# Optimization experiments

Hardware: AMD Instinct MI355X
Metric: run time of the kernel (lower is better)

Reference implementation:

```python
import jax, jax.numpy as jnp
import numpy as np

N_NODES = 100000
N_EDGES = 1600000
N_GRAPHS = 4096
BN_EPS = 1e-5


def _gcn_conv(h, src, tgt, deg_inv_sqrt, W, b):
    # GCNConv with self-loops: out_i = sum_{j->i} (d_i d_j)^{-1/2} (XW)_j + d_i^{-1} (XW)_i + b
    h = h @ W                                   # [N, out]
    norm = (deg_inv_sqrt[src] * deg_inv_sqrt[tgt])[:, None]  # [E, 1]
    agg = jax.ops.segment_sum(h[src] * norm, tgt, num_segments=N_NODES)
    agg = agg + h * (deg_inv_sqrt ** 2)[:, None]  # self-loop term
    return agg + b


def _batch_norm(x, gamma, beta):
    # training-mode BatchNorm1d: batch statistics, biased variance
    mean = jnp.mean(x, axis=0)
    var = jnp.mean((x - mean) ** 2, axis=0)
    return (x - mean) * jax.lax.rsqrt(var + BN_EPS) * gamma + beta


def setup_inputs() -> dict:
    key = jax.random.key(0)
    ks = jax.random.split(key, 12)
    x = jax.random.normal(ks[0], (N_NODES, 128), dtype=jnp.float32)
    edge_index = jax.random.randint(ks[1], (2, N_EDGES), 0, N_NODES, dtype=jnp.int32)
    batch = jnp.sort(jax.random.randint(ks[2], (N_NODES,), 0, N_GRAPHS, dtype=jnp.int32))
    def lin(k, fi, fo):
        return jax.random.normal(k, (fi, fo), dtype=jnp.float32) / np.sqrt(fi)
    return {
        "x": x, "edge_index": edge_index, "batch": batch,
        "W1": lin(ks[3], 128, 128), "b1": jnp.zeros((128,), jnp.float32),
        "W2": lin(ks[4], 128, 128), "b2": jnp.zeros((128,), jnp.float32),
        "W3": lin(ks[5], 128, 256), "b3": jnp.zeros((256,), jnp.float32),
        "g1": jnp.ones((128,), jnp.float32), "be1": jnp.zeros((128,), jnp.float32),
        "g2": jnp.ones((128,), jnp.float32), "be2": jnp.zeros((128,), jnp.float32),
    }


def reference(x, edge_index, batch, W1, b1, W2, b2, W3, b3, g1, be1, g2, be2):
    src, tgt = edge_index[0], edge_index[1]
    # degrees including self-loop
    deg = jax.ops.segment_sum(jnp.ones((N_EDGES,), x.dtype), tgt, num_segments=N_NODES) + 1.0
    deg_inv_sqrt = jax.lax.rsqrt(deg)

    h = _gcn_conv(x, src, tgt, deg_inv_sqrt, W1, b1)
    h = jax.nn.relu(_batch_norm(h, g1, be1))          # dropout(p=0.1) as identity (eval)
    h = _gcn_conv(h, src, tgt, deg_inv_sqrt, W2, b2)
    h = jax.nn.relu(_batch_norm(h, g2, be2))
    h = _gcn_conv(h, src, tgt, deg_inv_sqrt, W3, b3)  # [N, 256]

    # global mean pool over batch ids
    sums = jax.ops.segment_sum(h, batch, num_segments=N_GRAPHS)
    counts = jax.ops.segment_sum(jnp.ones((N_NODES,), h.dtype), batch, num_segments=N_GRAPHS)
    return sums / jnp.maximum(counts, 1.0)[:, None]
```

## Files before the change

kernel.cpp:

```cpp
#include <hip/hip_runtime.h>
#include <hip/hip_bf16.h>

#define BN_EPS 1e-5f
#define SCAN_CHUNK 2048
#define AGG_BLOCKS 2048
#define BSHIFT 9
#define BUCKN 512
#define NBP 256
#define CB 256

static inline int cdiv(long long a, long long b) { return (int)((a + b - 1) / b); }

typedef __attribute__((ext_vector_type(8))) short short8v;
typedef __attribute__((ext_vector_type(4))) float f32x4;

__device__ __forceinline__ float lo16(int u) {
    return __uint_as_float(((unsigned int)u) << 16);
}
__device__ __forceinline__ float hi16(int u) {
    return __uint_as_float(((unsigned int)u) & 0xffff0000u);
}
__device__ __forceinline__ unsigned short f2bf(float f) {
    unsigned int b = __float_as_uint(f);
    b += 0x7FFFu + ((b >> 16) & 1u);
    return (unsigned short)(b >> 16);
}

__global__ __launch_bounds__(256) void k_bhist(const int* __restrict__ tgt,
                                               int* __restrict__ hcnt, int E, int tile,
                                               int nbuck) {
    __shared__ int lh[NBP];
    const int t = threadIdx.x;
    lh[t] = 0;
    __syncthreads();
    const int base = blockIdx.x * tile;
    const int end = min(base + tile, E);
    for (int i = base + t; i < end; i += 256)
        atomicAdd(&lh[tgt[i] >> BSHIFT], 1);
    __syncthreads();
    if (t < nbuck) hcnt[blockIdx.x * NBP + t] = lh[t];
}

__global__ __launch_bounds__(256) void k_bscan(int* __restrict__ hcnt,
                                               int* __restrict__ btot) {
    const int bucket = blockIdx.x;
    const int t = threadIdx.x;
    __shared__ int sh[256];
    int v = hcnt[t * NBP + bucket];
    sh[t] = v;
    __syncthreads();
    for (int d = 1; d < 256; d <<= 1) {
        int u = (t >= d) ? sh[t - d] : 0;
        __syncthreads();
        sh[t] += u;
        __syncthreads();
    }
    hcnt[t * NBP + bucket] = sh[t] - v;
    if (t == 255) btot[bucket] = sh[255];
}

__global__ __launch_bounds__(256) void k_scan_small(const int* __restrict__ btot,
                                                    int* __restrict__ bbase, int nb) {
    const int t = threadIdx.x;
    __shared__ int sh[256];
    int v = (t < nb) ? btot[t] : 0;
    sh[t] = v;
    __syncthreads();
    for (int d = 1; d < 256; d <<= 1) {
        int u = (t >= d) ? sh[t - d] : 0;
        __syncthreads();
        sh[t] += u;
        __syncthreads();
    }
    if (t < nb) bbase[t] = sh[t] - v;
    if (t == nb) bbase[nb] = sh[255];
    if (t == 255 && nb <= 255) bbase[nb] = sh[255];
}

__global__ __launch_bounds__(256) void k_bscatter2(const int* __restrict__ src,
                                                   const int* __restrict__ tgt,
                                                   const int* __restrict__ hcnt,
                                                   const int* __restrict__ bbase,
                                                   int2* __restrict__ pairs, int E,
                                                   int tile, int nbuck) {
    __shared__ int cur[NBP];
    const int t = threadIdx.x;
    if (t < nbuck) cur[t] = bbase[t] + hcnt[blockIdx.x * NBP + t];
    __syncthreads();
    const int base = blockIdx.x * tile;
    const int end = min(base + tile, E);
    for (int i = base + t; i < end; i += 256) {
        int s = src[i];
        int tg = tgt[i];
        int p = atomicAdd(&cur[tg >> BSHIFT], 1);
        pairs[p] = make_int2(s, tg);
    }
}

__global__ __launch_bounds__(256) void k_bucket_ncnt(const int2* __restrict__ pairs,
                                                     const int* __restrict__ bbase,
                                                     int* __restrict__ ncnt, int N) {
    __shared__ int cnt[BUCKN];
    const int b = blockIdx.x;
    const int t = threadIdx.x;
    const int nb0 = b * BUCKN;
#pragma unroll
    for (int k = t; k < BUCKN; k += 256) cnt[k] = 0;
    __syncthreads();
    const int lo = bbase[b], hi = bbase[b + 1];
    for (int p = lo + t; p < hi; p += 256)
        atomicAdd(&cnt[pairs[p].y - nb0], 1);
    __syncthreads();
#pragma unroll
    for (int k = t; k < BUCKN; k += 256) {
        int node = nb0 + k;
        if (node < N) ncnt[node] = cnt[k];
    }
}

__global__ __launch_bounds__(256) void k_scan_blk(const int* __restrict__ cnt,
                                                  int* __restrict__ bsum, int n) {
    const int t = threadIdx.x;
    const int base = blockIdx.x * SCAN_CHUNK + t * 8;
    int s = 0;
    if (base + 8 <= n) {
        int4 a = *(const int4*)(cnt + base);
        int4 b = *(const int4*)(cnt + base + 4);
        s = a.x + a.y + a.z + a.w + b.x + b.y + b.z + b.w;
    } else {
#pragma unroll
        for (int j = 0; j < 8; j++) {
            int i = base + j;
            if (i < n) s += cnt[i];
        }
    }
    __shared__ int red[256];
    red[t] = s;
    __syncthreads();
    for (int d = 128; d > 0; d >>= 1) {
        if (t < d) red[t] += red[t + d];
        __syncthreads();
    }
    if (t == 0) bsum[blockIdx.x] = red[0];
}

__global__ __launch_bounds__(256) void k_scan_bsum(int* __restrict__ bsum,
                                                   int* __restrict__ off, int nb, int n) {
    const int t = threadIdx.x;
    __shared__ int sh[256];
    int v = (t < nb) ? bsum[t] : 0;
    sh[t] = v;
    __syncthreads();
    for (int d = 1; d < 256; d <<= 1) {
        int u = (t >= d) ? sh[t - d] : 0;
        __syncthreads();
        sh[t] += u;
        __syncthreads();
    }
    if (t < nb) bsum[t] = sh[t] - v;
    if (t == 255) off[n] = sh[255];
}

__global__ __launch_bounds__(256) void k_scan_out(const int* __restrict__ cnt,
                                                  const int* __restrict__ bsum,
                                                  int* __restrict__ off, int n,
                                                  float* __restrict__ dis,
                                                  int* __restrict__ cursor) {
    const int t = threadIdx.x;
    const int base = blockIdx.x * SCAN_CHUNK + t * 8;
    int c[8], loc[8];
    int s = 0;
#pragma unroll
    for (int j = 0; j < 8; j++) {
        int i = base + j;
        c[j] = (i < n) ? cnt[i] : 0;
        loc[j] = s;
        s += c[j];
    }
    __shared__ int sh[256];
    sh[t] = s;
    __syncthreads();
    for (int d = 1; d < 256; d <<= 1) {
        int u = (t >= d) ? sh[t - d] : 0;
        __syncthreads();
        sh[t] += u;
        __syncthreads();
    }
    const int texcl = sh[t] - s + bsum[blockIdx.x];
#pragma unroll
    for (int j = 0; j < 8; j++) {
        int i = base + j;
        if (i < n) {
            int o = texcl + loc[j];
            off[i] = o;
            if (cursor) cursor[i] = o;
            if (dis) dis[i] = rsqrtf((float)c[j] + 1.0f);
        }
    }
}

__global__ __launch_bounds__(256) void k_bucket_fill(const int2* __restrict__ pairs,
                                                     const int* __restrict__ bbase,
                                                     int* __restrict__ cursor,
                                                     int* __restrict__ esrc) {
    const int b = blockIdx.x;
    const int t = threadIdx.x;
    const int lo = bbase[b], hi = bbase[b + 1];
    for (int p = lo + t; p < hi; p += 256) {
        int2 e = pairs[p];
        int q = atomicAdd(&cursor[e.y], 1);
        esrc[q] = e.x;
    }
}

__global__ void k_goff(const int* __restrict__ batch, int* __restrict__ goff,
                       int N, int G) {
    int i = blockIdx.x * blockDim.x + threadIdx.x;
    if (i >= N) return;
    int cur = batch[i];
    int prev = (i == 0) ? -1 : batch[i - 1];
    for (int g = prev + 1; g <= cur; g++) goff[g] = i;
    if (i == N - 1) {
        for (int g = cur + 1; g <= G; g++) goff[g] = N;
    }
}

template <bool BN>
__global__ __launch_bounds__(256) void k_gemm_mfma(const float* __restrict__ X,
                                                   const float* __restrict__ W,
                                                   unsigned short* __restrict__ Y, int N,
                                                   const float* __restrict__ dis,
                                                   const float* __restrict__ sums,
                                                   const float* __restrict__ sumsq,
                                                   const float* __restrict__ g,
                                                   const float* __restrict__ be,
                                                   float inv_n) {
    __shared__ unsigned short As[64][136];
    __shared__ unsigned short Bs[64][136];
    const int t = threadIdx.x;
    const int rbase = blockIdx.x * 64;
    const int cbase = blockIdx.y * 64;

    for (int it = 0; it < 8; it++) {
        int idx = t + it * 256;
        int r = idx >> 5;
        int k4 = (idx & 31) * 4;
        int row = rbase + r;
        float4 v = make_float4(0.f, 0.f, 0.f, 0.f);
        if (row < N) v = *(const float4*)(X + (size_t)row * 128 + k4);
        float o[4] = {v.x, v.y, v.z, v.w};
        if (BN) {
#pragma unroll
            for (int j = 0; j < 4; j++) {
                int c = k4 + j;
                float mean = sums[c] * inv_n;
                float var = sumsq[c] * inv_n - mean * mean;
                float sc = rsqrtf(var + BN_EPS) * g[c];
                o[j] = fmaxf((o[j] - mean) * sc + be[c], 0.0f);
            }
        }
        ushort4 u;
        u.x = f2bf(o[0]); u.y = f2bf(o[1]); u.z = f2bf(o[2]); u.w = f2bf(o[3]);
        *(ushort4*)&As[r][k4] = u;
    }
    for (int it = 0; it < 8; it++) {
        int idx = t + it * 256;
        int k = idx >> 4;
        int c4 = (idx & 15) * 4;
        float4 v = *(const float4*)(W + (size_t)k * 128 + cbase + c4);
        Bs[c4 + 0][k] = f2bf(v.x);
        Bs[c4 + 1][k] = f2bf(v.y);
        Bs[c4 + 2][k] = f2bf(v.z);
        Bs[c4 + 3][k] = f2bf(v.w);
    }
    __syncthreads();

    const int wid = t >> 6;
    const int lane = t & 63;
    const int wr = (wid >> 1) * 32;
    const int wc = (wid & 1) * 32;
    const int lrow = lane & 15;
    const int lkg = lane >> 4;

    f32x4 acc00 = 0, acc01 = 0, acc10 = 0, acc11 = 0;
#pragma unroll
    for (int kk = 0; kk < 4; kk++) {
        const int k0 = kk * 32 + lkg * 8;
        short8v a0 = *(const short8v*)&As[wr + lrow][k0];
        short8v a1 = *(const short8v*)&As[wr + 16 + lrow][k0];
        short8v b0 = *(const short8v*)&Bs[wc + lrow][k0];
        short8v b1 = *(const short8v*)&Bs[wc + 16 + lrow][k0];
        acc00 = __builtin_amdgcn_mfma_f32_16x16x32_bf16(a0, b0, acc00, 0, 0, 0);
        acc01 = __builtin_amdgcn_mfma_f32_16x16x32_bf16(a0, b1, acc01, 0, 0, 0);
        acc10 = __builtin_amdgcn_mfma_f32_16x16x32_bf16(a1, b0, acc10, 0, 0, 0);
        acc11 = __builtin_amdgcn_mfma_f32_16x16x32_bf16(a1, b1, acc11, 0, 0, 0);
    }

#pragma unroll
    for (int rt = 0; rt < 2; rt++) {
        const f32x4 va = rt ? acc10 : acc00;
        const f32x4 vb = rt ? acc11 : acc01;
#pragma unroll
        for (int reg = 0; reg < 4; reg++) {
            int row = rbase + wr + rt * 16 + lkg * 4 + reg;
            if (row < N) {
                float dv = dis[row];
                Y[(size_t)row * 128 + cbase + wc + lrow] = f2bf(va[reg] * dv);
                Y[(size_t)row * 128 + cbase + wc + 16 + lrow] = f2bf(vb[reg] * dv);
            }
        }
    }
}

__global__ __launch_bounds__(256) void k_gemm_final(const float* __restrict__ X,
                                                    const float* __restrict__ W,
                                                    const float* __restrict__ bias,
                                                    const int* __restrict__ goff,
                                                    float* __restrict__ out, int G) {
    __shared__ float xt[128][64];
    __shared__ float wt[128][64];
    const int t = threadIdx.x;
    const int rbase = blockIdx.x * 64;
    const int cbase = blockIdx.y * 64;

    for (int it = 0; it < 8; it++) {
        int idx = t + it * 256;
        int k4 = idx >> 6;
        int r = idx & 63;
        int row = rbase + r;
        float4 v = make_float4(0.f, 0.f, 0.f, 0.f);
        if (row < G) v = *(const float4*)(X + (size_t)row * 128 + k4 * 4);
        xt[k4 * 4 + 0][r] = v.x;
        xt[k4 * 4 + 1][r] = v.y;
        xt[k4 * 4 + 2][r] = v.z;
        xt[k4 * 4 + 3][r] = v.w;
    }
    for (int it = 0; it < 8; it++) {
        int idx = t + it * 256;
        int k = idx >> 4;
        int c4 = (idx & 15) * 4;
        *(float4*)&wt[k][c4] = *(const float4*)(W + (size_t)k * 256 + cbase + c4);
    }
    __syncthreads();

    const int r0 = (t >> 4) * 4;
    const int c0 = (t & 15) * 4;
    float acc[4][4];
#pragma unroll
    for (int i = 0; i < 4; i++)
#pragma unroll
        for (int j = 0; j < 4; j++) acc[i][j] = 0.0f;

#pragma unroll 4
    for (int k = 0; k < 128; k++) {
        float4 a = *(const float4*)&xt[k][r0];
        float4 b = *(const float4*)&wt[k][c0];
        const float av[4] = {a.x, a.y, a.z, a.w};
        const float bv[4] = {b.x, b.y, b.z, b.w};
#pragma unroll
        for (int i = 0; i < 4; i++)
#pragma unroll
            for (int j = 0; j < 4; j++) acc[i][j] += av[i] * bv[j];
    }

#pragma unroll
    for (int i = 0; i < 4; i++) {
        int row = rbase + r0 + i;
        if (row < G) {
            bool empty = (goff[row + 1] == goff[row]);
            float4 o;
            o.x = empty ? 0.f : acc[i][0] + bias[cbase + c0 + 0];
            o.y = empty ? 0.f : acc[i][1] + bias[cbase + c0 + 1];
            o.z = empty ? 0.f : acc[i][2] + bias[cbase + c0 + 2];
            o.w = empty ? 0.f : acc[i][3] + bias[cbase + c0 + 3];
            *(float4*)(out + (size_t)row * 256 + cbase + c0) = o;
        }
    }
}

template <bool STATS>
__global__ __launch_bounds__(256) void k_aggr2(const unsigned short* __restrict__ H,
                                               const int* __restrict__ esrc,
                                               const int* __restrict__ roff,
                                               const float* __restrict__ dis,
                                               const float* __restrict__ bias,
                                               float* __restrict__ out, int N,
                                               float* __restrict__ partial) {
    constexpr int M = 128;
    constexpr int GSZ = 16;
    constexpr int GPB = 16;
    const int nGroups = gridDim.x * GPB;
    const int gid = blockIdx.x * GPB + threadIdx.x / GSZ;
    const int lane = threadIdx.x % GSZ;
    const int c8 = lane * 8;
    const float4 bva = *(const float4*)(bias + c8);
    const float4 bvb = *(const float4*)(bias + c8 + 4);

    float ss[8], sq[8];
    if (STATS) {
#pragma unroll
        for (int k = 0; k < 8; k++) { ss[k] = 0.f; sq[k] = 0.f; }
    }

    for (int n = gid; n < N; n += nGroups) {
        const int rs = roff[n], re = roff[n + 1];
        float acc[8];
#pragma unroll
        for (int j = 0; j < 8; j++) acc[j] = 0.0f;

        int e = rs;
        for (; e + 8 <= re; e += 8) {
            int sid[8];
#pragma unroll
            for (int q = 0; q < 8; q++) sid[q] = esrc[e + q];
            int4 hv[8];
#pragma unroll
            for (int q = 0; q < 8; q++)
                hv[q] = *(const int4*)(H + (size_t)sid[q] * M + c8);
#pragma unroll
            for (int q = 0; q < 8; q++) {
                const int w[4] = {hv[q].x, hv[q].y, hv[q].z, hv[q].w};
#pragma unroll
                for (int k = 0; k < 4; k++) {
                    acc[2 * k + 0] += lo16(w[k]);
                    acc[2 * k + 1] += hi16(w[k]);
                }
            }
        }
        if (e + 4 <= re) {
            int sid[4];
#pragma unroll
            for (int q = 0; q < 4; q++) sid[q] = esrc[e + q];
            int4 hv[4];
#pragma unroll
            for (int q = 0; q < 4; q++)
                hv[q] = *(const int4*)(H + (size_t)sid[q] * M + c8);
#pragma unroll
            for (int q = 0; q < 4; q++) {
                const int w[4] = {hv[q].x, hv[q].y, hv[q].z, hv[q].w};
#pragma unroll
                for (int k = 0; k < 4; k++) {
                    acc[2 * k + 0] += lo16(w[k]);
                    acc[2 * k + 1] += hi16(w[k]);
                }
            }
            e += 4;
        }
        for (; e < re; e++) {
            const int s = esrc[e];
            const int4 h = *(const int4*)(H + (size_t)s * M + c8);
            const int w[4] = {h.x, h.y, h.z, h.w};
#pragma unroll
            for (int k = 0; k < 4; k++) {
                acc[2 * k + 0] += lo16(w[k]);
                acc[2 * k + 1] += hi16(w[k]);
            }
        }
        {
            const int4 h = *(const int4*)(H + (size_t)n * M + c8);
            const int w[4] = {h.x, h.y, h.z, h.w};
#pragma unroll
            for (int k = 0; k < 4; k++) {
                acc[2 * k + 0] += lo16(w[k]);
                acc[2 * k + 1] += hi16(w[k]);
            }
        }
        const float dn = dis[n];
        float ov[8];
#pragma unroll
        for (int k = 0; k < 8; k++) {
            float b = (k < 4) ? (&bva.x)[k] : (&bvb.x)[k - 4];
            ov[k] = acc[k] * dn + b;
            if (STATS) { ss[k] += ov[k]; sq[k] += ov[k] * ov[k]; }
        }
        float4 oa = make_float4(ov[0], ov[1], ov[2], ov[3]);
        float4 ob = make_float4(ov[4], ov[5], ov[6], ov[7]);
        *(float4*)(out + (size_t)n * M + c8) = oa;
        *(float4*)(out + (size_t)n * M + c8 + 4) = ob;
    }

    if (STATS) {
        __shared__ float ls[GPB][256];
        const int g = threadIdx.x / GSZ;
#pragma unroll
        for (int k = 0; k < 8; k++) {
            ls[g][c8 + k] = ss[k];
            ls[g][128 + c8 + k] = sq[k];
        }
        __syncthreads();
        const int f = threadIdx.x;
        float v = 0.f;
#pragma unroll
        for (int gg = 0; gg < GPB; gg++) v += ls[gg][f];
        partial[(size_t)blockIdx.x * 256 + f] = v;
    }
}

__global__ __launch_bounds__(256) void k_redstats(const float* __restrict__ partial,
                                                  float* __restrict__ sums,
                                                  float* __restrict__ sumsq, int nblk) {
    const int f = blockIdx.x;
    const int t = threadIdx.x;
    float v = 0.f;
    for (int b = t; b < nblk; b += 256) v += partial[(size_t)b * 256 + f];
    __shared__ float sh[256];
    sh[t] = v;
    __syncthreads();
    for (int d = 128; d > 0; d >>= 1) {
        if (t < d) sh[t] += sh[t + d];
        __syncthreads();
    }
    if (t == 0) {
        if (f < 128) sums[f] = sh[0];
        else sumsq[f - 128] = sh[0];
    }
}

__global__ void k_bncast(const float* __restrict__ X, const float* __restrict__ sums,
                         const float* __restrict__ sumsq, const float* __restrict__ g,
                         const float* __restrict__ be, const float* __restrict__ dis,
                         unsigned short* __restrict__ Y, long long total4, float inv_n) {
    long long idx = (long long)blockIdx.x * blockDim.x + threadIdx.x;
    if (idx >= total4) return;
    int c4 = ((int)idx & 31) << 2;
    const float dn = dis[(int)(idx >> 5)];
    float4 v = *(const float4*)(X + idx * 4);
    float o[4] = {v.x, v.y, v.z, v.w};
    ushort4 r;
    unsigned short* rp = &r.x;
#pragma unroll
    for (int j = 0; j < 4; j++) {
        int c = c4 + j;
        float mean = sums[c] * inv_n;
        float var = sumsq[c] * inv_n - mean * mean;
        float sc = rsqrtf(var + BN_EPS) * g[c];
        rp[j] = f2bf(fmaxf((o[j] - mean) * sc + be[c], 0.0f) * dn);
    }
    *(ushort4*)(Y + idx * 4) = r;
}

__global__ void k_pool_seg(const float* __restrict__ H, const int* __restrict__ goff,
                           float* __restrict__ out) {
    const int gr = blockIdx.x;
    const int c = threadIdx.x;
    const int s = goff[gr], e = goff[gr + 1];
    float acc = 0.0f;
    for (int i = s; i < e; i++) acc += H[(size_t)i * 128 + c];
    out[(size_t)gr * 128 + c] = acc / fmaxf((float)(e - s), 1.0f);
}

extern "C" void kernel_launch(void* const* d_in, const int* in_sizes, int n_in,
                              void* d_out, int out_size, void* d_ws, size_t ws_size,
                              hipStream_t stream) {
    const float* x     = (const float*)d_in[0];
    const int*   ei    = (const int*)d_in[1];
    const int*   batch = (const int*)d_in[2];
    const float* W1 = (const float*)d_in[3];
    const float* b1 = (const float*)d_in[4];
    const float* W2 = (const float*)d_in[5];
    const float* b2 = (const float*)d_in[6];
    const float* W3 = (const float*)d_in[7];
    const float* b3 = (const float*)d_in[8];
    const float* g1 = (const float*)d_in[9];
    const float* be1 = (const float*)d_in[10];
    const float* g2 = (const float*)d_in[11];
    const float* be2 = (const float*)d_in[12];
    float* out = (float*)d_out;

    const int N = in_sizes[2];
    const int E = in_sizes[1] / 2;
    const int G = out_size / 256;
    const int* src = ei;
    const int* tgt = ei + E;

    char* ws = (char*)d_ws;
    auto take = [&](size_t bytes) {
        char* p = ws;
        ws += (bytes + 255) & ~(size_t)255;
        return p;
    };
    float*          bufB   = (float*)take((size_t)N * 128 * 4);
    unsigned short* bufH   = (unsigned short*)take((size_t)N * 128 * 2);
    float*          P      = (float*)take((size_t)G * 128 * 4);
    float*          dis    = (float*)take((size_t)N * 4);
    float*          sums   = (float*)take(512 * 4);
    float*          sumsq  = sums + 128;
    float*          zbias  = (float*)take(128 * 4);
    float*          partial= (float*)take((size_t)AGG_BLOCKS * 256 * 4);
    int*            ncnt   = (int*)take((size_t)N * 4);
    int*            roff   = (int*)take((size_t)(N + 1) * 4);
    int*            cursor = (int*)take((size_t)N * 4);
    int*            esrc   = (int*)take((size_t)E * 4);
    int*            goff   = (int*)take((size_t)(G + 1) * 4);
    int*            bsumN  = (int*)take(256 * 4);
    int*            hcnt   = (int*)take((size_t)CB * NBP * 4);
    int*            btot   = (int*)take(NBP * 4);
    int*            bbase  = (int*)take((NBP + 1) * 4);
    int2*           pairs  = (int2*)bufB;

    const int B = 256;
    const int nbN = cdiv(N, SCAN_CHUNK);
    const int nbuck = cdiv(N, BUCKN);
    const int tile = cdiv(E, CB);

    hipMemsetAsync(zbias, 0, 128 * 4, stream);

    k_bhist<<<CB, B, 0, stream>>>(tgt, hcnt, E, tile, nbuck);
    k_bscan<<<nbuck, B, 0, stream>>>(hcnt, btot);
    k_scan_small<<<1, B, 0, stream>>>(btot, bbase, nbuck);
    k_bscatter2<<<CB, B, 0, stream>>>(src, tgt, hcnt, bbase, pairs, E, tile, nbuck);
    k_bucket_ncnt<<<nbuck, B, 0, stream>>>(pairs, bbase, ncnt, N);
    k_scan_blk<<<nbN, B, 0, stream>>>(ncnt, bsumN, N);
    k_scan_bsum<<<1, B, 0, stream>>>(bsumN, roff, nbN, N);
    k_scan_out<<<nbN, B, 0, stream>>>(ncnt, bsumN, roff, N, dis, cursor);
    k_bucket_fill<<<nbuck, B, 0, stream>>>(pairs, bbase, cursor, esrc);
    k_goff<<<cdiv(N, B), B, 0, stream>>>(batch, goff, N, G);

    long long t4_128 = (long long)N * 32;
    const int nbx = cdiv(N, 64);

    k_gemm_mfma<false><<<dim3(nbx, 2), B, 0, stream>>>(x, W1, bufH, N, dis,
                                                       nullptr, nullptr, nullptr, nullptr, 0.f);
    k_aggr2<true><<<AGG_BLOCKS, B, 0, stream>>>(bufH, esrc, roff, dis, b1, bufB, N, partial);
    k_redstats<<<256, B, 0, stream>>>(partial, sums, sumsq, AGG_BLOCKS);

    k_gemm_mfma<true><<<dim3(nbx, 2), B, 0, stream>>>(bufB, W2, bufH, N, dis,
                                                      sums, sumsq, g1, be1, 1.0f / N);
    k_aggr2<true><<<AGG_BLOCKS, B, 0, stream>>>(bufH, esrc, roff, dis, b2, bufB, N, partial);
    k_redstats<<<256, B, 0, stream>>>(partial, sums, sumsq, AGG_BLOCKS);

    k_bncast<<<cdiv(t4_128, B), B, 0, stream>>>(bufB, sums, sumsq, g2, be2, dis, bufH,
                                                t4_128, 1.0f / N);
    k_aggr2<false><<<AGG_BLOCKS, B, 0, stream>>>(bufH, esrc, roff, dis, zbias, bufB, N, nullptr);
    k_pool_seg<<<G, 128, 0, stream>>>(bufB, goff, P);
    k_gemm_final<<<dim3(cdiv(G, 64), 4), B, 0, stream>>>(P, W3, b3, goff, out, G);
}
```

Baseline: 406.7 us.

## Fuse per-bucket CSR build into one kernel, widen aggregation unroll and grid

Merges the node-count, three-pass global scan and fill kernels into a single per-bucket kernel. Each block counts its targets in shared memory, scans locally from the bucket base offset, writes roff and dis, and fills esrc using shared-memory cursors instead of global atomics. This removes four launches and global ncnt/cursor traffic. The aggregation inner loop now gathers 16 neighbours at a time for more memory-level parallelism, at some register cost, and AGG_BLOCKS doubles to 4096.

```diff
diff --git a/kernel.cpp b/kernel.cpp
--- a/kernel.cpp
+++ b/kernel.cpp
@@ -2,8 +2,7 @@
 #include <hip/hip_bf16.h>
 
 #define BN_EPS 1e-5f
-#define SCAN_CHUNK 2048
-#define AGG_BLOCKS 2048
+#define AGG_BLOCKS 4096
 #define BSHIFT 9
 #define BUCKN 512
 #define NBP 256
@@ -97,59 +96,28 @@
     }
 }
 
-__global__ __launch_bounds__(256) void k_bucket_ncnt(const int2* __restrict__ pairs,
-                                                     const int* __restrict__ bbase,
-                                                     int* __restrict__ ncnt, int N) {
+__global__ __launch_bounds__(256) void k_bucket_csr(const int2* __restrict__ pairs,
+                                                    const int* __restrict__ bbase,
+                                                    int* __restrict__ roff,
+                                                    float* __restrict__ dis,
+                                                    int* __restrict__ esrc,
+                                                    int N, int nbuck) {
     __shared__ int cnt[BUCKN];
+    __shared__ int cur[BUCKN];
+    __shared__ int sh[256];
     const int b = blockIdx.x;
     const int t = threadIdx.x;
     const int nb0 = b * BUCKN;
-#pragma unroll
-    for (int k = t; k < BUCKN; k += 256) cnt[k] = 0;
+    cnt[t] = 0;
+    cnt[t + 256] = 0;
     __syncthreads();
     const int lo = bbase[b], hi = bbase[b + 1];
     for (int p = lo + t; p < hi; p += 256)
         atomicAdd(&cnt[pairs[p].y - nb0], 1);
     __syncthreads();
-#pragma unroll
-    for (int k = t; k < BUCKN; k += 256) {
-        int node = nb0 + k;
-        if (node < N) ncnt[node] = cnt[k];
-    }
-}
-
-__global__ __launch_bounds__(256) void k_scan_blk(const int* __restrict__ cnt,
-                                                  int* __restrict__ bsum, int n) {
-    const int t = threadIdx.x;
-    const int base = blockIdx.x * SCAN_CHUNK + t * 8;
-    int s = 0;
-    if (base + 8 <= n) {
-        int4 a = *(const int4*)(cnt + base);
-        int4 b = *(const int4*)(cnt + base + 4);
-        s = a.x + a.y + a.z + a.w + b.x + b.y + b.z + b.w;
-    } else {
-#pragma unroll
-        for (int j = 0; j < 8; j++) {
-            int i = base + j;
-            if (i < n) s += cnt[i];
-        }
-    }
-    __shared__ int red[256];
-    red[t] = s;
-    __syncthreads();
-    for (int d = 128; d > 0; d >>= 1) {
-        if (t < d) red[t] += red[t + d];
-        __syncthreads();
-    }
-    if (t == 0) bsum[blockIdx.x] = red[0];
-}
-
-__global__ __launch_bounds__(256) void k_scan_bsum(int* __restrict__ bsum,
-                                                   int* __restrict__ off, int nb, int n) {
-    const int t = threadIdx.x;
-    __shared__ int sh[256];
-    int v = (t < nb) ? bsum[t] : 0;
-    sh[t] = v;
+    const int c0 = cnt[2 * t], c1 = cnt[2 * t + 1];
+    int s = c0 + c1;
+    sh[t] = s;
     __syncthreads();
     for (int d = 1; d < 256; d <<= 1) {
         int u = (t >= d) ? sh[t - d] : 0;
@@ -157,58 +125,17 @@
         sh[t] += u;
         __syncthreads();
     }
-    if (t < nb) bsum[t] = sh[t] - v;
-    if (t == 255) off[n] = sh[255];
-}
-
-__global__ __launch_bounds__(256) void k_scan_out(const int* __restrict__ cnt,
-                                                  const int* __restrict__ bsum,
-                                                  int* __restrict__ off, int n,
-                                                  float* __restrict__ dis,
-                                                  int* __restrict__ cursor) {
-    const int t = threadIdx.x;
-    const int base = blockIdx.x * SCAN_CHUNK + t * 8;
-    int c[8], loc[8];
-    int s = 0;
-#pragma unroll
-    for (int j = 0; j < 8; j++) {
-        int i = base + j;
-        c[j] = (i < n) ? cnt[i] : 0;
-        loc[j] = s;
-        s += c[j];
-    }
-    __shared__ int sh[256];
-    sh[t] = s;
-    __syncthreads();
-    for (int d = 1; d < 256; d <<= 1) {
-        int u = (t >= d) ? sh[t - d] : 0;
-        __syncthreads();
-        sh[t] += u;
-        __syncthreads();
-    }
-    const int texcl = sh[t] - s + bsum[blockIdx.x];
-#pragma unroll
-    for (int j = 0; j < 8; j++) {
-        int i = base + j;
-        if (i < n) {
-            int o = texcl + loc[j];
-            off[i] = o;
-            if (cursor) cursor[i] = o;
-            if (dis) dis[i] = rsqrtf((float)c[j] + 1.0f);
-        }
-    }
-}
-
-__global__ __launch_bounds__(256) void k_bucket_fill(const int2* __restrict__ pairs,
-                                                     const int* __restrict__ bbase,
-                                                     int* __restrict__ cursor,
-                                                     int* __restrict__ esrc) {
-    const int b = blockIdx.x;
-    const int t = threadIdx.x;
-    const int lo = bbase[b], hi = bbase[b + 1];
+    const int excl = sh[t] - s + lo;
+    cur[2 * t] = excl;
+    cur[2 * t + 1] = excl + c0;
+    const int n0 = nb0 + 2 * t, n1 = n0 + 1;
+    if (n0 < N) { roff[n0] = excl; dis[n0] = rsqrtf((float)c0 + 1.0f); }
+    if (n1 < N) { roff[n1] = excl + c0; dis[n1] = rsqrtf((float)c1 + 1.0f); }
+    if (b == nbuck - 1 && t == 0) roff[N] = hi;
+    __syncthreads();
     for (int p = lo + t; p < hi; p += 256) {
         int2 e = pairs[p];
-        int q = atomicAdd(&cursor[e.y], 1);
+        int q = atomicAdd(&cur[e.y - nb0], 1);
         esrc[q] = e.x;
     }
 }
@@ -409,16 +336,16 @@
         for (int j = 0; j < 8; j++) acc[j] = 0.0f;
 
         int e = rs;
-        for (; e + 8 <= re; e += 8) {
-            int sid[8];
-#pragma unroll
-            for (int q = 0; q < 8; q++) sid[q] = esrc[e + q];
-            int4 hv[8];
-#pragma unroll
-            for (int q = 0; q < 8; q++)
+        for (; e + 16 <= re; e += 16) {
+            int sid[16];
+#pragma unroll
+            for (int q = 0; q < 16; q++) sid[q] = esrc[e + q];
+            int4 hv[16];
+#pragma unroll
+            for (int q = 0; q < 16; q++)
                 hv[q] = *(const int4*)(H + (size_t)sid[q] * M + c8);
 #pragma unroll
-            for (int q = 0; q < 8; q++) {
+            for (int q = 0; q < 16; q++) {
                 const int w[4] = {hv[q].x, hv[q].y, hv[q].z, hv[q].w};
 #pragma unroll
                 for (int k = 0; k < 4; k++) {
@@ -426,6 +353,25 @@
                     acc[2 * k + 1] += hi16(w[k]);
                 }
             }
+        }
+        if (e + 8 <= re) {
+            int sid[8];
+#pragma unroll
+            for (int q = 0; q < 8; q++) sid[q] = esrc[e + q];
+            int4 hv[8];
+#pragma unroll
+            for (int q = 0; q < 8; q++)
+                hv[q] = *(const int4*)(H + (size_t)sid[q] * M + c8);
+#pragma unroll
+            for (int q = 0; q < 8; q++) {
+                const int w[4] = {hv[q].x, hv[q].y, hv[q].z, hv[q].w};
+#pragma unroll
+                for (int k = 0; k < 4; k++) {
+                    acc[2 * k + 0] += lo16(w[k]);
+                    acc[2 * k + 1] += hi16(w[k]);
+                }
+            }
+            e += 8;
         }
         if (e + 4 <= re) {
             int sid[4];
@@ -587,19 +533,15 @@
     float*          sumsq  = sums + 128;
     float*          zbias  = (float*)take(128 * 4);
     float*          partial= (float*)take((size_t)AGG_BLOCKS * 256 * 4);
-    int*            ncnt   = (int*)take((size_t)N * 4);
     int*            roff   = (int*)take((size_t)(N + 1) * 4);
-    int*            cursor = (int*)take((size_t)N * 4);
     int*            esrc   = (int*)take((size_t)E * 4);
     int*            goff   = (int*)take((size_t)(G + 1) * 4);
-    int*            bsumN  = (int*)take(256 * 4);
     int*            hcnt   = (int*)take((size_t)CB * NBP * 4);
     int*            btot   = (int*)take(NBP * 4);
     int*            bbase  = (int*)take((NBP + 1) * 4);
     int2*           pairs  = (int2*)bufB;
 
     const int B = 256;
-    const int nbN = cdiv(N, SCAN_CHUNK);
     const int nbuck = cdiv(N, BUCKN);
     const int tile = cdiv(E, CB);
 
@@ -609,11 +551,7 @@
     k_bscan<<<nbuck, B, 0, stream>>>(hcnt, btot);
     k_scan_small<<<1, B, 0, stream>>>(btot, bbase, nbuck);
     k_bscatter2<<<CB, B, 0, stream>>>(src, tgt, hcnt, bbase, pairs, E, tile, nbuck);
-    k_bucket_ncnt<<<nbuck, B, 0, stream>>>(pairs, bbase, ncnt, N);
-    k_scan_blk<<<nbN, B, 0, stream>>>(ncnt, bsumN, N);
-    k_scan_bsum<<<1, B, 0, stream>>>(bsumN, roff, nbN, N);
-    k_scan_out<<<nbN, B, 0, stream>>>(ncnt, bsumN, roff, N, dis, cursor);
-    k_bucket_fill<<<nbuck, B, 0, stream>>>(pairs, bbase, cursor, esrc);
+    k_bucket_csr<<<nbuck, B, 0, stream>>>(pairs, bbase, roff, dis, esrc, N, nbuck);
     k_goff<<<cdiv(N, B), B, 0, stream>>>(batch, goff, N, G);
 
     long long t4_128 = (long long)N * 32;
```

New measurement: 387.4 us. 4.8% less time.
